# Optimization experiments

Hardware: AMD Instinct MI355X
Metric: run time of the kernel (lower is better)

Reference implementation:

```python
import jax, jax.numpy as jnp
import numpy as np

EPS = 1e-5
L0_BETA = 2.0 / 3.0   # unused in deterministic path
L0_GAMMA = -0.1
L0_ZETA = 1.1
NEG_SLOPE = 0.2


def _bn(v, axes, g, b, pshape):
    # batch-norm using batch statistics (training-mode math, biased var like torch)
    mean = jnp.mean(v, axis=axes, keepdims=True)
    var = jnp.var(v, axis=axes, keepdims=True)
    return (v - mean) * jax.lax.rsqrt(var + EPS) * g.reshape(pshape) + b.reshape(pshape)


def setup_inputs() -> dict:
    key = jax.random.key(0)
    ks = jax.random.split(key, 4)
    n, c, t, h, w = 32, 1024, 32, 7, 7
    n_nodes = 128
    return {
        "x": jax.random.normal(ks[0], (n, c, t, h, w), jnp.float32),
        "nodes": jax.random.normal(ks[1], (n_nodes, c), jnp.float32),
        "g1": jnp.ones((c,), jnp.float32), "b1": jnp.zeros((c,), jnp.float32),
        "g2": jnp.ones((c,), jnp.float32), "b2": jnp.zeros((c,), jnp.float32),
        "g3": jnp.ones((n_nodes,), jnp.float32), "b3": jnp.zeros((n_nodes,), jnp.float32),
        "W": jax.random.normal(ks[2], (c, c), jnp.float32) * (1.0 / np.sqrt(c)),
        "bW": jnp.zeros((c,), jnp.float32),
        "loc": jnp.ones((1,), jnp.float32),  # hard-concrete location param (penalty_loc_mean=1)
        "g6": jnp.ones((c,), jnp.float32), "b6": jnp.zeros((c,), jnp.float32),
    }


def reference(x, nodes, g1, b1, g2, b2, g3, b3, W, bW, loc, g6, b6):
    # x: (n,c,t,h,w), nodes: (K,c)
    # bn_1: BatchNorm3d over channel c
    x = _bn(x, (0, 2, 3, 4), g1, b1, (1, -1, 1, 1, 1))
    # bn_2: BatchNorm1d on (K,c) -> per-channel stats across nodes
    nd = _bn(nodes, (0,), g2, b2, (1, -1))
    # linear_1
    nd = nd @ W.T + bW
    # bn_3: pl.BatchNorm(n_nodes, dim=0) -> per-node stats across channels
    nd = _bn(nd, (1,), g3, b3, (-1, 1))
    # tensor_product_1: f (n,h,w,K,t)
    f = jnp.einsum('ncthw,kc->nhwkt', x, nd)
    # L0Norm hard-concrete gate (deterministic/eval path)
    s_bar = jax.nn.sigmoid(loc) * (L0_ZETA - L0_GAMMA) + L0_GAMMA
    gate = jnp.clip(s_bar, 0.0, 1.0)
    alpha = f * gate
    # tensor_product_2: y (n,c,t,h,w)
    y = jnp.einsum('nhwkt,kc->ncthw', alpha, nd)
    # bn_6 + LeakyReLU(0.2)
    y = _bn(y, (0, 2, 3, 4), g6, b6, (1, -1, 1, 1, 1))
    return jnp.where(y >= 0, y, NEG_SLOPE * y)
```

## Files before the change

### kernel.cpp

```cpp
#include <hip/hip_runtime.h>
#include <hip/hip_bf16.h>

#define NB 32
#define CC 1024
#define SS 1568
#define KK 128
#define NCOL 448
#define EPSV 1e-5f
#define XP_P 132
#define NSB3 224

typedef __attribute__((ext_vector_type(8))) short bf16x8;
typedef __attribute__((ext_vector_type(4))) short bf16x4v;
typedef __attribute__((ext_vector_type(4))) float f32x4;

__device__ __forceinline__ unsigned short f2bf(float f) {
  union { float f; unsigned u; } v; v.f = f;
  return (unsigned short)((v.u + 0x7fffu + ((v.u >> 16) & 1u)) >> 16);
}
__device__ __forceinline__ float bf2f(unsigned short h) {
  union { unsigned u; float f; } v; v.u = ((unsigned)h) << 16; return v.f;
}

__global__ __launch_bounds__(512) void xpose_stats(
    const float* __restrict__ x, unsigned short* __restrict__ xT,
    float* __restrict__ p1s, float* __restrict__ p1q) {
  __shared__ float lt[64 * XP_P];
  int sb = blockIdx.x, cc = blockIdx.y, n = blockIdx.z;
  int t = threadIdx.x;
  int s0 = sb * 112, c0 = cc * 64;
  const float* xp = x + ((size_t)n * CC + c0) * SS + s0;
  #pragma unroll
  for (int j = 0; j < 4; j++) {
    int idx = t + 512 * j;
    if (idx < 1792) {
      int r = idx / 28, q = idx % 28;
      float4 v = *(const float4*)(xp + (size_t)r * SS + 4 * q);
      *(float4*)&lt[r * XP_P + 4 * (q ^ (r >> 3))] = v;
    }
  }
  __syncthreads();
  if (t < 256) {
    int r = t >> 2, m = t & 3;
    float s = 0.f, sq = 0.f;
    #pragma unroll
    for (int i = 0; i < 7; i++) {
      int b = m * 7 + i;
      float4 v = *(const float4*)&lt[r * XP_P + 4 * (b ^ (r >> 3))];
      s  += v.x + v.y + v.z + v.w;
      sq += v.x * v.x + v.y * v.y + v.z * v.z + v.w * v.w;
    }
    s += __shfl_xor(s, 1); sq += __shfl_xor(sq, 1);
    s += __shfl_xor(s, 2); sq += __shfl_xor(sq, 2);
    if (m == 0) {
      int col = n * 14 + sb;
      p1s[(size_t)(c0 + r) * NCOL + col] = s;
      p1q[(size_t)(c0 + r) * NCOL + col] = sq;
    }
  }
  if (t < 448) {
    int co = t & 7, sl = t >> 3;
    #pragma unroll
    for (int j = 0; j < 2; j++) {
      int sloc = sl + 56 * j;
      int s = s0 + sloc;
      bf16x8 pk;
      #pragma unroll
      for (int i = 0; i < 8; i++) {
        int r = co * 8 + i;
        pk[i] = (short)f2bf(lt[r * XP_P + 4 * ((sloc >> 2) ^ co) + (sloc & 3)]);
      }
      size_t off = (size_t)n * 1605632 +
                   (size_t)((s >> 4) * 32 + (cc * 2 + (co >> 2))) * 512 +
                   (s & 15) * 32 + (co & 3) * 8;
      *(bf16x8*)(xT + off) = pk;
    }
  }
}

__global__ void prep_stats(const float* __restrict__ nodes, const float* __restrict__ g2,
                           const float* __restrict__ b2, unsigned short* __restrict__ nh,
                           const float* __restrict__ p1s, const float* __restrict__ p1q,
                           const float* __restrict__ g1, const float* __restrict__ b1,
                           float* a1, float* c1) {
  __shared__ float sred[4][8][2];
  __shared__ float bc[8][2];
  __shared__ float red1[4][32][2];
  int t = threadIdx.x, w = t >> 6;
  if (blockIdx.x < 128) {
    int blk = blockIdx.x;
    int cl = t & 7, kq = t >> 3;
    int c = blk * 8 + cl;
    float s = 0.f, sq = 0.f;
    #pragma unroll
    for (int i = 0; i < 4; i++) {
      float v = nodes[(size_t)(kq + 32 * i) * CC + c];
      s += v; sq += v * v;
    }
    s += __shfl_xor(s, 8);  sq += __shfl_xor(sq, 8);
    s += __shfl_xor(s, 16); sq += __shfl_xor(sq, 16);
    s += __shfl_xor(s, 32); sq += __shfl_xor(sq, 32);
    if ((t & 63) < 8) { sred[w][cl][0] = s; sred[w][cl][1] = sq; }
    __syncthreads();
    if (t < 8) {
      float st = sred[0][t][0] + sred[1][t][0] + sred[2][t][0] + sred[3][t][0];
      float qt = sred[0][t][1] + sred[1][t][1] + sred[2][t][1] + sred[3][t][1];
      float inv = 1.f / (float)KK;
      float m = st * inv, var = qt * inv - m * m;
      float r = rsqrtf(var + EPSV);
      float a = g2[blk * 8 + t] * r;
      bc[t][0] = a; bc[t][1] = b2[blk * 8 + t] - m * a;
    }
    __syncthreads();
    float a = bc[cl][0], cc2 = bc[cl][1];
    #pragma unroll
    for (int i = 0; i < 4; i++) {
      int k = kq + 32 * i;
      nh[(size_t)k * CC + c] = f2bf(nodes[(size_t)k * CC + c] * a + cc2);
    }
  } else {
    int blk = blockIdx.x - 128;
    int cl = t & 31, part = t >> 5;
    int c = blk * 32 + cl;
    const float4* ps = (const float4*)(p1s + (size_t)c * NCOL + part * 56);
    const float4* pq = (const float4*)(p1q + (size_t)c * NCOL + part * 56);
    float s = 0.f, sq = 0.f;
    #pragma unroll
    for (int i = 0; i < 14; i++) {
      float4 v = ps[i]; s += v.x + v.y + v.z + v.w;
      float4 u = pq[i]; sq += u.x + u.y + u.z + u.w;
    }
    s += __shfl_xor(s, 32); sq += __shfl_xor(sq, 32);
    if ((t & 63) < 32) { red1[w][cl][0] = s; red1[w][cl][1] = sq; }
    __syncthreads();
    if (t < 32) {
      float st = red1[0][t][0] + red1[1][t][0] + red1[2][t][0] + red1[3][t][0];
      float qt = red1[0][t][1] + red1[1][t][1] + red1[2][t][1] + red1[3][t][1];
      float inv = 1.f / ((float)NB * SS);
      float m = st * inv, var = qt * inv - m * m;
      float r = rsqrtf(var + EPSV);
      float a = g1[c] * r;
      a1[c] = a; c1[c] = b1[c] - m * a;
    }
  }
}

__global__ __launch_bounds__(256) void linear_mfma(
    const unsigned short* __restrict__ nh, const float* __restrict__ Wm,
    const float* __restrict__ bW, float* __restrict__ Lb) {
  int jt = blockIdx.x, mt = blockIdx.y;
  int t = threadIdx.x, w = t >> 6, lane = t & 63, g = lane >> 4, l15 = lane & 15;
  int krow = mt * 64 + w * 16 + l15;
  f32x4 acc[2];
  acc[0] = (f32x4){0.f,0.f,0.f,0.f}; acc[1] = (f32x4){0.f,0.f,0.f,0.f};
  #pragma unroll 4
  for (int c0 = 0; c0 < CC; c0 += 32) {
    bf16x8 af = *(const bf16x8*)(nh + (size_t)krow * CC + c0 + g * 8);
    #pragma unroll
    for (int nf = 0; nf < 2; nf++) {
      const float* wr = Wm + (size_t)(jt * 32 + nf * 16 + l15) * CC + c0 + g * 8;
      float4 v0 = *(const float4*)wr, v1 = *(const float4*)(wr + 4);
      bf16x8 bfr;
      bfr[0] = (short)f2bf(v0.x); bfr[1] = (short)f2bf(v0.y);
      bfr[2] = (short)f2bf(v0.z); bfr[3] = (short)f2bf(v0.w);
      bfr[4] = (short)f2bf(v1.x); bfr[5] = (short)f2bf(v1.y);
      bfr[6] = (short)f2bf(v1.z); bfr[7] = (short)f2bf(v1.w);
      acc[nf] = __builtin_amdgcn_mfma_f32_16x16x32_bf16(af, bfr, acc[nf], 0, 0, 0);
    }
  }
  #pragma unroll
  for (int nf = 0; nf < 2; nf++) {
    int j = jt * 32 + nf * 16 + l15;
    float bwv = bW[j];
    #pragma unroll
    for (int r = 0; r < 4; r++)
      Lb[(size_t)(mt * 64 + w * 16 + g * 4 + r) * CC + j] = acc[nf][r] + bwv;
  }
}

__global__ void bn3_pack(const float* __restrict__ Lb, const float* __restrict__ g3,
                         const float* __restrict__ b3, const float* __restrict__ loc,
                         const float* __restrict__ a1, const float* __restrict__ c1,
                         unsigned short* __restrict__ ndA2, unsigned short* __restrict__ Mt,
                         unsigned short* __restrict__ MtL, float* __restrict__ Cst) {
  __shared__ float red[8];
  int k = blockIdx.x, t = threadIdx.x, w = t >> 6;
  float vv[4];
  float s = 0.f, sq = 0.f;
  for (int i = 0; i < 4; i++) {
    float v = Lb[(size_t)k * CC + t + 256 * i];
    vv[i] = v; s += v; sq += v * v;
  }
  for (int m = 1; m < 64; m <<= 1) { s += __shfl_xor(s, m); sq += __shfl_xor(sq, m); }
  if ((t & 63) == 0) { red[w] = s; red[4 + w] = sq; }
  __syncthreads();
  s  = red[0] + red[1] + red[2] + red[3];
  sq = red[4] + red[5] + red[6] + red[7];
  float inv = 1.f / (float)CC;
  float m3 = s * inv, var = sq * inv - m3 * m3;
  float r = rsqrtf(var + EPSV);
  float a = g3[k] * r, cc3 = b3[k] - m3 * a;
  float lv = loc[0];
  float gate = 1.f / (1.f + __expf(-lv)) * 1.2f - 0.1f;
  gate = fminf(fmaxf(gate, 0.f), 1.f);
  float cs = 0.f;
  for (int i = 0; i < 4; i++) {
    int j = t + 256 * i;
    float nd = vv[i] * a + cc3;
    unsigned short ndb = f2bf(nd * a1[j]);
    unsigned short mtb = f2bf(gate * nd);
    ndA2[(size_t)((k >> 4) * 32 + (j >> 5)) * 512 + (k & 15) * 32 + ((j >> 3) & 3) * 8 + (j & 7)] = ndb;
    Mt[(size_t)((j >> 4) * 4 + (k >> 5)) * 512 + (j & 15) * 32 + ((k >> 3) & 3) * 8 + (k & 7)] = mtb;
    MtL[(size_t)j * KK + k] = mtb;
    cs += c1[j] * nd;
  }
  for (int m = 1; m < 64; m <<= 1) cs += __shfl_xor(cs, m);
  __syncthreads();
  if ((t & 63) == 0) red[w] = cs;
  __syncthreads();
  if (t == 0) Cst[k] = red[0] + red[1] + red[2] + red[3];
}

__global__ __launch_bounds__(256) void gemm1(
    const unsigned short* __restrict__ ndA2, const unsigned short* __restrict__ xT,
    const float* __restrict__ Cst, unsigned short* __restrict__ GT) {
  int sb = blockIdx.x;
  int n  = blockIdx.y;
  int t = threadIdx.x, w = t >> 6, lane = t & 63, g = lane >> 4, l15 = lane & 15;
  f32x4 acc[2][2];
  for (int m = 0; m < 2; m++)
    for (int nf = 0; nf < 2; nf++) acc[m][nf] = (f32x4){0.f, 0.f, 0.f, 0.f};
  int lofs = l15 * 32 + g * 8;
  const unsigned short* xb = xT + (size_t)n * 1605632;
  #pragma unroll 4
  for (int cc2 = 0; cc2 < 32; cc2++) {
    bf16x8 af[2], bfr[2];
    #pragma unroll
    for (int m = 0; m < 2; m++)
      af[m] = *(const bf16x8*)(ndA2 + (size_t)((w * 2 + m) * 32 + cc2) * 512 + lofs);
    #pragma unroll
    for (int nf = 0; nf < 2; nf++)
      bfr[nf] = *(const bf16x8*)(xb + (size_t)((sb * 2 + nf) * 32 + cc2) * 512 + lofs);
    #pragma unroll
    for (int m = 0; m < 2; m++)
      #pragma unroll
      for (int nf = 0; nf < 2; nf++)
        acc[m][nf] = __builtin_amdgcn_mfma_f32_16x16x32_bf16(af[m], bfr[nf], acc[m][nf], 0, 0, 0);
  }
  unsigned short* gtn = GT + (size_t)n * 200704;
  #pragma unroll
  for (int nf = 0; nf < 2; nf++) {
    #pragma unroll
    for (int m = 0; m < 2; m++) {
      int kb = w * 32 + m * 16 + g * 4;
      float4 cst = *(const float4*)(Cst + kb);
      bf16x4v ov;
      ov[0] = (short)f2bf(acc[m][nf][0] + cst.x);
      ov[1] = (short)f2bf(acc[m][nf][1] + cst.y);
      ov[2] = (short)f2bf(acc[m][nf][2] + cst.z);
      ov[3] = (short)f2bf(acc[m][nf][3] + cst.w);
      int g2 = m * 2 + (g >> 1);
      int e0 = (g & 1) * 4;
      *(bf16x4v*)(gtn + (size_t)((sb * 2 + nf) * 4 + w) * 512 + l15 * 32 + g2 * 8 + e0) = ov;
    }
  }
}

__global__ __launch_bounds__(256) void gram(const unsigned short* __restrict__ GT,
                                            float* __restrict__ part) {
  __shared__ float lf[112 * 128];
  int b = blockIdx.x, t = threadIdx.x;
  int k1b = t >> 4, k2b = t & 15;
  float acc[8][8];
  float gsum[8];
  #pragma unroll
  for (int i = 0; i < 8; i++) {
    gsum[i] = 0.f;
    #pragma unroll
    for (int j = 0; j < 8; j++) acc[i][j] = 0.f;
  }
  for (int chunk = 0; chunk < 2; chunk++) {
    int St0 = b * 14 + chunk * 7;
    #pragma unroll
    for (int it = 0; it < 7; it++) {
      int u = t + 256 * it;
      int Stl = u >> 8, rem = u & 255;
      bf16x8 v = *(const bf16x8*)(GT + (size_t)(St0 + Stl) * 2048 + rem * 8);
      int sl = Stl * 16 + ((rem & 63) >> 2);
      int kk = (rem >> 6) * 32 + (rem & 3) * 8;
      float4 f0, f1;
      f0.x = bf2f((unsigned short)v[0]); f0.y = bf2f((unsigned short)v[1]);
      f0.z = bf2f((unsigned short)v[2]); f0.w = bf2f((unsigned short)v[3]);
      f1.x = bf2f((unsigned short)v[4]); f1.y = bf2f((unsigned short)v[5]);
      f1.z = bf2f((unsigned short)v[6]); f1.w = bf2f((unsigned short)v[7]);
      *(float4*)&lf[sl * 128 + kk] = f0;
      *(float4*)&lf[sl * 128 + kk + 4] = f1;
    }
    __syncthreads();
    for (int sl = 0; sl < 112; sl++) {
      float4 a0 = *(const float4*)&lf[sl * 128 + k1b * 8];
      float4 a1 = *(const float4*)&lf[sl * 128 + k1b * 8 + 4];
      float4 b0 = *(const float4*)&lf[sl * 128 + k2b * 8];
      float4 b1 = *(const float4*)&lf[sl * 128 + k2b * 8 + 4];
      float a[8]  = {a0.x, a0.y, a0.z, a0.w, a1.x, a1.y, a1.z, a1.w};
      float bb[8] = {b0.x, b0.y, b0.z, b0.w, b1.x, b1.y, b1.z, b1.w};
      #pragma unroll
      for (int i = 0; i < 8; i++)
        #pragma unroll
        for (int j = 0; j < 8; j++) acc[i][j] += a[i] * bb[j];
      if (k1b == 0) {
        #pragma unroll
        for (int j = 0; j < 8; j++) gsum[j] += bb[j];
      }
    }
    __syncthreads();
  }
  float* pb = part + (size_t)b * 16512;
  #pragma unroll
  for (int i = 0; i < 8; i++) {
    int k1 = k1b * 8 + i;
    *(float4*)(pb + k1 * 128 + k2b * 8)     = (float4){acc[i][0], acc[i][1], acc[i][2], acc[i][3]};
    *(float4*)(pb + k1 * 128 + k2b * 8 + 4) = (float4){acc[i][4], acc[i][5], acc[i][6], acc[i][7]};
  }
  if (k1b == 0) {
    *(float4*)(pb + 16384 + k2b * 8)     = (float4){gsum[0], gsum[1], gsum[2], gsum[3]};
    *(float4*)(pb + 16384 + k2b * 8 + 4) = (float4){gsum[4], gsum[5], gsum[6], gsum[7]};
  }
}

__global__ void gram_reduceA(const float* __restrict__ part, float* __restrict__ partB) {
  int e = blockIdx.x * 256 + threadIdx.x;
  if (e >= 16512) return;
  int p0 = blockIdx.y * 56;
  float s = 0.f;
  #pragma unroll 8
  for (int p = p0; p < p0 + 56; p++) s += part[(size_t)p * 16512 + e];
  partB[(size_t)blockIdx.y * 16512 + e] = s;
}

__global__ __launch_bounds__(256) void bn6stats(
    const float* __restrict__ partB, const unsigned short* __restrict__ MtL,
    const float* __restrict__ g6, const float* __restrict__ b6,
    float* a6, float* c6) {
  __shared__ float covL[16384];
  __shared__ float mL[8 * 128];
  __shared__ float gbL[128];
  int b = blockIdx.x, t = threadIdx.x;
  int c0 = b * 8;
  #pragma unroll
  for (int i = 0; i < 16; i++) {
    int u = (t + 256 * i) * 4;
    float4 va = *(const float4*)(partB + u);
    float4 vb = *(const float4*)(partB + 16512 + u);
    float4 vc = *(const float4*)(partB + 2 * 16512 + u);
    float4 vd = *(const float4*)(partB + 3 * 16512 + u);
    *(float4*)&covL[u] = (float4){va.x + vb.x + vc.x + vd.x, va.y + vb.y + vc.y + vd.y,
                                  va.z + vb.z + vc.z + vd.z, va.w + vb.w + vc.w + vd.w};
  }
  if (t < 128) {
    int row = t >> 4, unit = t & 15;
    bf16x8 v = *(const bf16x8*)(MtL + (size_t)(c0 + row) * KK + unit * 8);
    #pragma unroll
    for (int j = 0; j < 8; j++) mL[row * 128 + unit * 8 + j] = bf2f((unsigned short)v[j]);
  }
  if (t < 32) {
    int u = 16384 + t * 4;
    float4 va = *(const float4*)(partB + u);
    float4 vb = *(const float4*)(partB + 16512 + u);
    float4 vc = *(const float4*)(partB + 2 * 16512 + u);
    float4 vd = *(const float4*)(partB + 3 * 16512 + u);
    *(float4*)&gbL[t * 4] = (float4){va.x + vb.x + vc.x + vd.x, va.y + vb.y + vc.y + vd.y,
                                     va.z + vb.z + vc.z + vd.z, va.w + vb.w + vc.w + vd.w};
  }
  __syncthreads();
  int cl = t >> 5, kq = t & 31;
  float4 m4 = *(const float4*)&mL[cl * 128 + kq * 4];
  float4 g4 = *(const float4*)&gbL[kq * 4];
  float mv = m4.x * g4.x + m4.y * g4.y + m4.z * g4.z + m4.w * g4.w;
  float vv = 0.f;
  for (int k = 0; k < 128; k++) {
    float4 c4 = *(const float4*)&covL[k * 128 + kq * 4];
    float mk = mL[cl * 128 + k];
    vv += mk * (c4.x * m4.x + c4.y * m4.y + c4.z * m4.z + c4.w * m4.w);
  }
  for (int msk = 1; msk < 32; msk <<= 1) { mv += __shfl_xor(mv, msk); vv += __shfl_xor(vv, msk); }
  if (kq == 0) {
    int c = c0 + cl;
    float inv = 1.f / ((float)NB * SS);
    float mean = mv * inv, var = vv * inv - mean * mean;
    float r = rsqrtf(var + EPSV);
    float a = g6[c] * r;
    a6[c] = a; c6[c] = b6[c] - mean * a;
  }
}

__global__ __launch_bounds__(256) void gemm2(
    const unsigned short* __restrict__ Mt, const unsigned short* __restrict__ GT,
    const float* __restrict__ a6, const float* __restrict__ c6,
    float* __restrict__ out) {
  int id = blockIdx.x;
  int xcd = id & 7;
  int mid = id >> 3;
  int ct  = mid & 7;
  int p   = (mid >> 3) * 8 + xcd;
  int sb  = p % 14, n = p / 14;
  int t = threadIdx.x, w = t >> 6, lane = t & 63, g = lane >> 4, l15 = lane & 15;
  f32x4 acc[2][7];
  for (int m = 0; m < 2; m++)
    for (int nf = 0; nf < 7; nf++) acc[m][nf] = (f32x4){0.f, 0.f, 0.f, 0.f};
  int lofs = l15 * 32 + g * 8;
  const unsigned short* gtb = GT + (size_t)n * 200704;
  #pragma unroll
  for (int ks = 0; ks < 4; ks++) {
    bf16x8 af[2];
    #pragma unroll
    for (int m = 0; m < 2; m++)
      af[m] = *(const bf16x8*)(Mt + (size_t)((ct * 8 + w * 2 + m) * 4 + ks) * 512 + lofs);
    #pragma unroll
    for (int nf = 0; nf < 7; nf++) {
      bf16x8 bfr = *(const bf16x8*)(gtb + (size_t)((sb * 7 + nf) * 4 + ks) * 512 + lofs);
      #pragma unroll
      for (int m = 0; m < 2; m++)
        acc[m][nf] = __builtin_amdgcn_mfma_f32_16x16x32_bf16(af[m], bfr, acc[m][nf], 0, 0, 0);
    }
  }
  #pragma unroll
  for (int m = 0; m < 2; m++) {
    int cb = ct * 128 + w * 32 + m * 16 + g * 4;
    float4 av = *(const float4*)(a6 + cb);
    float4 cv = *(const float4*)(c6 + cb);
    #pragma unroll
    for (int nf = 0; nf < 7; nf++) {
      int s = sb * 112 + nf * 16 + l15;
      #pragma unroll
      for (int r = 0; r < 4; r++) {
        float a = (r == 0) ? av.x : (r == 1) ? av.y : (r == 2) ? av.z : av.w;
        float cc = (r == 0) ? cv.x : (r == 1) ? cv.y : (r == 2) ? cv.z : cv.w;
        float v = acc[m][nf][r] * a + cc;
        v = v >= 0.f ? v : 0.2f * v;
        __builtin_nontemporal_store(v, &out[((size_t)(n * CC + cb + r)) * SS + s]);
      }
    }
  }
}

extern "C" void kernel_launch(void* const* d_in, const int* in_sizes, int n_in,
                              void* d_out, int out_size, void* d_ws, size_t ws_size,
                              hipStream_t stream) {
  const float* x     = (const float*)d_in[0];
  const float* nodes = (const float*)d_in[1];
  const float* g1 = (const float*)d_in[2];
  const float* b1 = (const float*)d_in[3];
  const float* g2 = (const float*)d_in[4];
  const float* b2 = (const float*)d_in[5];
  const float* g3 = (const float*)d_in[6];
  const float* b3 = (const float*)d_in[7];
  const float* Wm = (const float*)d_in[8];
  const float* bW = (const float*)d_in[9];
  const float* loc = (const float*)d_in[10];
  const float* g6 = (const float*)d_in[11];
  const float* b6 = (const float*)d_in[12];
  float* out = (float*)d_out;
  char* ws = (char*)d_ws;

  float* p1s = (float*)(ws + 0);
  float* p1q = (float*)(ws + 1835008);
  float* a1  = (float*)(ws + 3670016);
  float* c1  = (float*)(ws + 3674112);
  float* Cst = (float*)(ws + 3678208);
  unsigned short* nh   = (unsigned short*)(ws + 3682304);
  float* Lb  = (float*)(ws + 3944448);
  unsigned short* ndA2 = (unsigned short*)(ws + 4468736);
  unsigned short* Mt   = (unsigned short*)(ws + 4730880);
  unsigned short* MtL  = (unsigned short*)(ws + 4993024);
  float* a6  = (float*)(ws + 5255168);
  float* c6  = (float*)(ws + 5259264);
  float* gramP = (float*)(ws + 5329920);
  unsigned short* GT = (unsigned short*)(ws + 20124672);
  unsigned short* xT = (unsigned short*)(ws + 32969728);
  float* partB = (float*)(ws + 135730176);

  xpose_stats<<<dim3(14, 16, NB), dim3(512), 0, stream>>>(x, xT, p1s, p1q);
  prep_stats<<<dim3(160), dim3(256), 0, stream>>>(nodes, g2, b2, nh, p1s, p1q, g1, b1, a1, c1);
  linear_mfma<<<dim3(32, 2), dim3(256), 0, stream>>>(nh, Wm, bW, Lb);
  bn3_pack<<<dim3(KK), dim3(256), 0, stream>>>(Lb, g3, b3, loc, a1, c1, ndA2, Mt, MtL, Cst);
  gemm1<<<dim3(49, NB), dim3(256), 0, stream>>>(ndA2, xT, Cst, GT);
  gram<<<dim3(NSB3), dim3(256), 0, stream>>>(GT, gramP);
  gram_reduceA<<<dim3(65, 4), dim3(256), 0, stream>>>(gramP, partB);
  bn6stats<<<dim3(128), dim3(256), 0, stream>>>(partB, MtL, g6, b6, a6, c6);
  gemm2<<<dim3(3584), dim3(256), 0, stream>>>(Mt, GT, a6, c6, out);
}
```

Measured before the change: 274.4 us.

## Swap MFMA operands in gemm2 for vectorized output stores; rebalance xpose_stats work

In gemm2 the MFMA A/B operands are swapped so each lane holds four consecutive spatial outputs for one channel. The epilogue can then write one 16-byte nontemporal store per lane instead of four scalar strided stores, cutting the number of store instructions on the large fp32 output write. In xpose_stats the stats are now computed by the 64 otherwise idle threads (t>=448), one row each, running alongside the transpose threads instead of using a shuffle reduction over 256 threads. The gemm1 unroll factor is raised from 4 to 8, which may increase register pressure.

```diff
diff --git a/kernel.cpp b/kernel.cpp
--- a/kernel.cpp
+++ b/kernel.cpp
@@ -40,25 +40,19 @@
     }
   }
   __syncthreads();
-  if (t < 256) {
-    int r = t >> 2, m = t & 3;
+  if (t >= 448) {
+    int r = t - 448;
     float s = 0.f, sq = 0.f;
     #pragma unroll
-    for (int i = 0; i < 7; i++) {
-      int b = m * 7 + i;
+    for (int b = 0; b < 28; b++) {
       float4 v = *(const float4*)&lt[r * XP_P + 4 * (b ^ (r >> 3))];
       s  += v.x + v.y + v.z + v.w;
       sq += v.x * v.x + v.y * v.y + v.z * v.z + v.w * v.w;
     }
-    s += __shfl_xor(s, 1); sq += __shfl_xor(sq, 1);
-    s += __shfl_xor(s, 2); sq += __shfl_xor(sq, 2);
-    if (m == 0) {
-      int col = n * 14 + sb;
-      p1s[(size_t)(c0 + r) * NCOL + col] = s;
-      p1q[(size_t)(c0 + r) * NCOL + col] = sq;
-    }
-  }
-  if (t < 448) {
+    int col = n * 14 + sb;
+    p1s[(size_t)(c0 + r) * NCOL + col] = s;
+    p1q[(size_t)(c0 + r) * NCOL + col] = sq;
+  } else {
     int co = t & 7, sl = t >> 3;
     #pragma unroll
     for (int j = 0; j < 2; j++) {
@@ -232,7 +226,7 @@
     for (int nf = 0; nf < 2; nf++) acc[m][nf] = (f32x4){0.f, 0.f, 0.f, 0.f};
   int lofs = l15 * 32 + g * 8;
   const unsigned short* xb = xT + (size_t)n * 1605632;
-  #pragma unroll 4
+  #pragma unroll 8
   for (int cc2 = 0; cc2 < 32; cc2++) {
     bf16x8 af[2], bfr[2];
     #pragma unroll
@@ -405,9 +399,9 @@
   int p   = (mid >> 3) * 8 + xcd;
   int sb  = p % 14, n = p / 14;
   int t = threadIdx.x, w = t >> 6, lane = t & 63, g = lane >> 4, l15 = lane & 15;
-  f32x4 acc[2][7];
-  for (int m = 0; m < 2; m++)
-    for (int nf = 0; nf < 7; nf++) acc[m][nf] = (f32x4){0.f, 0.f, 0.f, 0.f};
+  f32x4 acc[7][2];
+  for (int nf = 0; nf < 7; nf++)
+    for (int m = 0; m < 2; m++) acc[nf][m] = (f32x4){0.f, 0.f, 0.f, 0.f};
   int lofs = l15 * 32 + g * 8;
   const unsigned short* gtb = GT + (size_t)n * 200704;
   #pragma unroll
@@ -421,25 +415,32 @@
       bf16x8 bfr = *(const bf16x8*)(gtb + (size_t)((sb * 7 + nf) * 4 + ks) * 512 + lofs);
       #pragma unroll
       for (int m = 0; m < 2; m++)
-        acc[m][nf] = __builtin_amdgcn_mfma_f32_16x16x32_bf16(af[m], bfr, acc[m][nf], 0, 0, 0);
-    }
-  }
+        acc[nf][m] = __builtin_amdgcn_mfma_f32_16x16x32_bf16(bfr, af[m], acc[nf][m], 0, 0, 0);
+    }
+  }
+  float a_[2], cc_[2];
+  size_t rowbase[2];
   #pragma unroll
   for (int m = 0; m < 2; m++) {
-    int cb = ct * 128 + w * 32 + m * 16 + g * 4;
-    float4 av = *(const float4*)(a6 + cb);
-    float4 cv = *(const float4*)(c6 + cb);
-    #pragma unroll
-    for (int nf = 0; nf < 7; nf++) {
-      int s = sb * 112 + nf * 16 + l15;
-      #pragma unroll
-      for (int r = 0; r < 4; r++) {
-        float a = (r == 0) ? av.x : (r == 1) ? av.y : (r == 2) ? av.z : av.w;
-        float cc = (r == 0) ? cv.x : (r == 1) ? cv.y : (r == 2) ? cv.z : cv.w;
-        float v = acc[m][nf][r] * a + cc;
-        v = v >= 0.f ? v : 0.2f * v;
-        __builtin_nontemporal_store(v, &out[((size_t)(n * CC + cb + r)) * SS + s]);
-      }
+    int c = ct * 128 + w * 32 + m * 16 + l15;
+    a_[m] = a6[c]; cc_[m] = c6[c];
+    rowbase[m] = ((size_t)(n * CC + c)) * SS;
+  }
+  #pragma unroll
+  for (int nf = 0; nf < 7; nf++) {
+    int s4 = sb * 112 + nf * 16 + g * 4;
+    #pragma unroll
+    for (int m = 0; m < 2; m++) {
+      f32x4 ov;
+      float v0 = acc[nf][m][0] * a_[m] + cc_[m];
+      float v1 = acc[nf][m][1] * a_[m] + cc_[m];
+      float v2 = acc[nf][m][2] * a_[m] + cc_[m];
+      float v3 = acc[nf][m][3] * a_[m] + cc_[m];
+      ov[0] = v0 >= 0.f ? v0 : 0.2f * v0;
+      ov[1] = v1 >= 0.f ? v1 : 0.2f * v1;
+      ov[2] = v2 >= 0.f ? v2 : 0.2f * v2;
+      ov[3] = v3 >= 0.f ? v3 : 0.2f * v3;
+      __builtin_nontemporal_store(ov, (f32x4*)&out[rowbase[m] + s4]);
     }
   }
 }
```

Result: slower. 286.2 us (+4.3%).
